# Optimization experiments

Hardware: AMD Instinct MI355X
Metric: run time of the kernel (lower is better)

## Reference

```python
import math
import jax, jax.numpy as jnp
import numpy as np

TOPK = 10
GAMMA = 0.0
DELTA = 0.05
EPS = 1e-8
QR_RANK_EPS = 1e-6
B, D, C = 4096, 2048, 10000


def setup_inputs() -> dict:
    key = jax.random.key(0)
    kz, kw, kn = jax.random.split(key, 3)
    z = jax.random.normal(kz, (B, D), jnp.float32)
    W = jax.random.normal(kw, (C, D), jnp.float32) * 0.02
    logits = z @ W.T                      # (B, C)
    y = jnp.argmax(logits, axis=1)        # correct-class labels -> positive margins
    noise = jax.random.normal(kn, (B, D), jnp.float32)  # one Gaussian draw per sample
    return {"z": z, "y": y, "logits": logits, "W": W, "noise": noise}


def reference(z, y, logits, W, noise):
    # z: (B,D), y: (B,), logits: (B,C), W: (C,D), noise: (B,D)
    b, d = z.shape
    c = W.shape[0]
    k = min(TOPK, c - 1)
    log_term = math.log(1.0 / max(DELTA, 1e-12))

    # top-K confusing classes (exclude true class)
    lm = logits.at[jnp.arange(b), y].set(-1e9)
    _, topk_idx = jax.lax.top_k(lm, k)            # (B, K)

    w_y = W[y]                                    # (B, D)
    w_ks = W[topk_idx]                            # (B, K, D)
    A = w_y[:, None, :] - w_ks                    # (B, K, D) rows = w_y - w_k

    # batched reduced QR of A^T : Q (B,D,K), R (B,K,K)
    Q, R = jnp.linalg.qr(jnp.swapaxes(A, 1, 2))
    keep = jnp.abs(jnp.diagonal(R, axis1=-2, axis2=-1)) > QR_RANK_EPS  # (B, K)
    Qm = Q * keep[:, None, :].astype(Q.dtype)     # zero dropped columns == Q[:, keep]
    valid_basis = keep.any(axis=1)

    # margins and nuisance-projected differences
    margins = jnp.einsum('bkd,bd->bk', A, z)                      # (B, K)
    coef = jnp.einsum('bkd,bdr->bkr', A, Qm)                      # (B, K, K)
    diffs_N = A - jnp.einsum('bkr,bdr->bkd', coef, Qm)            # (B, K, D)
    pn2 = jnp.maximum(jnp.sum(diffs_N * diffs_N, axis=-1), EPS)   # (B, K)
    slack = jnp.maximum(margins - GAMMA, 0.0)
    alpha_k = slack * slack / (2.0 * pn2 * log_term + EPS)
    alpha = jnp.min(alpha_k, axis=1)                              # (B,)

    valid = valid_basis & (alpha > 0.0) & jnp.isfinite(alpha)
    scale = jnp.where(valid, jnp.sqrt(jnp.maximum(alpha, 0.0)), 0.0)

    # project noise onto nuisance subspace and inject
    nc = jnp.einsum('bd,bdr->br', noise, Qm)
    epsN = noise - jnp.einsum('br,bdr->bd', nc, Qm)               # (B, D)
    z_aug = z + jax.lax.stop_gradient(scale[:, None] * epsN)
    # invalid samples carry scale=0 (z_aug == z); `valid` marks real augmentations
    return z_aug, y, valid
```

## Files before the change

### kernel.cpp

```cpp
#include <hip/hip_runtime.h>
#include <math.h>

#define BB 4096
#define DD 2048
#define CC 10000
#define KK 10
#define NT 256
#define NW 4
#define NF4 2500
#define TRI(k) ((k)*((k)+1)/2)

__global__ __launch_bounds__(NT, 6) void topk_kernel(
    const float* __restrict__ logits, const int* __restrict__ y,
    int* __restrict__ topk)
{
    __shared__ float s_cv[NW * KK];
    __shared__ int   s_ci[NW * KK];

    const int b = blockIdx.x, tid = threadIdx.x;
    const int lane = tid & 63, wave = tid >> 6;
    const int yb = y[b];

    float4 lg[10];
    const float4* lrow = (const float4*)(logits + (size_t)b * CC);
    #pragma unroll
    for (int j = 0; j < 10; ++j) {
        const int i4 = tid + 256 * j;
        if (i4 < NF4) lg[j] = lrow[i4];
        else          lg[j] = make_float4(-3e38f, -3e38f, -3e38f, -3e38f);
    }
    #pragma unroll
    for (int j = 0; j < 10; ++j) {
        const int rel = yb - 4 * (tid + 256 * j);
        if (rel == 0) lg[j].x = -3e38f;
        else if (rel == 1) lg[j].y = -3e38f;
        else if (rel == 2) lg[j].z = -3e38f;
        else if (rel == 3) lg[j].w = -3e38f;
    }

    float lbest; int lbidx;
    auto rescan = [&]() {
        lbest = -3.1e38f; lbidx = 0x7fffffff;
        #pragma unroll
        for (int j = 0; j < 10; ++j) {
            const int base = 4 * (tid + 256 * j);
            if (lg[j].x > lbest) { lbest = lg[j].x; lbidx = base + 0; }
            if (lg[j].y > lbest) { lbest = lg[j].y; lbidx = base + 1; }
            if (lg[j].z > lbest) { lbest = lg[j].z; lbidx = base + 2; }
            if (lg[j].w > lbest) { lbest = lg[j].w; lbidx = base + 3; }
        }
    };
    rescan();

    for (int r = 0; r < KK; ++r) {
        float bv = lbest; int bi = lbidx;
        #pragma unroll
        for (int off = 32; off > 0; off >>= 1) {
            const float ov = __shfl_down(bv, off, 64);
            const int   oi = __shfl_down(bi, off, 64);
            if (ov > bv || (ov == bv && oi < bi)) { bv = ov; bi = oi; }
        }
        bv = __shfl(bv, 0, 64);
        bi = __shfl(bi, 0, 64);
        if (lane == 0) { s_cv[wave * KK + r] = bv; s_ci[wave * KK + r] = bi; }
        if (lbidx == bi) {
            const int jw = ((bi >> 2) - tid) >> 8;
            const int cw = bi & 3;
            #pragma unroll
            for (int j = 0; j < 10; ++j) if (j == jw) {
                if (cw == 0) lg[j].x = -3e38f;
                else if (cw == 1) lg[j].y = -3e38f;
                else if (cw == 2) lg[j].z = -3e38f;
                else lg[j].w = -3e38f;
            }
            rescan();
        }
    }
    __syncthreads();

    if (wave == 0) {
        float cv = (lane < NW * KK) ? s_cv[lane] : -3.1e38f;
        int   ci = (lane < NW * KK) ? s_ci[lane] : 0x7fffffff;
        for (int r = 0; r < KK; ++r) {
            float bv = cv; int bi = ci;
            #pragma unroll
            for (int off = 32; off > 0; off >>= 1) {
                const float ov = __shfl_down(bv, off, 64);
                const int   oi = __shfl_down(bi, off, 64);
                if (ov > bv || (ov == bv && oi < bi)) { bv = ov; bi = oi; }
            }
            bi = __shfl(bi, 0, 64);
            if (lane == 0) topk[b * KK + r] = bi;
            if (ci == bi) cv = -3.1e38f;
        }
    }
}

__global__ __launch_bounds__(NT, 3) void aug_kernel(
    const float* __restrict__ z, const int* __restrict__ y,
    const float* __restrict__ W, const float* __restrict__ noise,
    const int* __restrict__ topk, float* __restrict__ out, int write_tail)
{
    __shared__ float s_part[NW][80];
    __shared__ float s_sol[16];

    const int b = blockIdx.x, tid = threadIdx.x;
    const int lane = tid & 63, wave = tid >> 6;
    const int yb = y[b];

    int kidx[KK];
    #pragma unroll
    for (int k = 0; k < KK; ++k) kidx[k] = topk[b * KK + k];

    const size_t zoff = (size_t)b * DD;
    const float4 z0 = ((const float4*)(z + zoff))[tid];
    const float4 z1 = ((const float4*)(z + zoff + 1024))[tid];
    const float4 n0 = ((const float4*)(noise + zoff))[tid];
    const float4 n1 = ((const float4*)(noise + zoff + 1024))[tid];

    float acc[75];
    #pragma unroll
    for (int t = 0; t < 75; ++t) acc[t] = 0.0f;

    const size_t wyo = (size_t)yb * DD;
    #pragma unroll
    for (int c = 0; c < 2; ++c) {
        const size_t coff = (size_t)c * 1024;
        const float4 wy4 = ((const float4*)(W + wyo + coff))[tid];
        float4 a4[KK];
        #pragma unroll
        for (int k = 0; k < KK; ++k) {
            const float4 wk4 = ((const float4*)(W + (size_t)kidx[k] * DD + coff))[tid];
            a4[k].x = wy4.x - wk4.x; a4[k].y = wy4.y - wk4.y;
            a4[k].z = wy4.z - wk4.z; a4[k].w = wy4.w - wk4.w;
        }
        const float4 zc = c ? z1 : z0;
        const float4 nc = c ? n1 : n0;
        const float ze[4] = {zc.x, zc.y, zc.z, zc.w};
        const float ne[4] = {nc.x, nc.y, nc.z, nc.w};
        #pragma unroll
        for (int e = 0; e < 4; ++e) {
            float ak[KK];
            #pragma unroll
            for (int k = 0; k < KK; ++k)
                ak[k] = (e == 0) ? a4[k].x : (e == 1) ? a4[k].y : (e == 2) ? a4[k].z : a4[k].w;
            #pragma unroll
            for (int k = 0; k < KK; ++k) {
                acc[55 + k] += ak[k] * ze[e];
                acc[65 + k] += ak[k] * ne[e];
                #pragma unroll
                for (int j = 0; j <= k; ++j)
                    acc[TRI(k) + j] += ak[j] * ak[k];
            }
        }
    }

    #pragma unroll
    for (int t = 0; t < 75; ++t) {
        float x = acc[t];
        #pragma unroll
        for (int off = 32; off > 0; off >>= 1) x += __shfl_down(x, off, 64);
        if (lane == 0) s_part[wave][t] = x;
    }
    __syncthreads();

    if (wave == 0) {
        float g[75];
        #pragma unroll
        for (int t = 0; t < 75; ++t)
            g[t] = s_part[0][t] + s_part[1][t] + s_part[2][t] + s_part[3][t];

        float dinv[KK];
        unsigned keepmask = 0u;
        #pragma unroll
        for (int k = 0; k < KK; ++k) {
            float s = g[TRI(k) + k];
            #pragma unroll
            for (int j = 0; j < KK; ++j) if (j < k) { const float l = g[TRI(k) + j]; s -= l * l; }
            const float dkk = sqrtf(fmaxf(s, 0.0f));
            const bool kp = dkk > 1e-6f;
            if (kp) keepmask |= (1u << k);
            dinv[k] = kp ? 1.0f / dkk : 0.0f;
            g[TRI(k) + k] = dkk;
            #pragma unroll
            for (int i = 0; i < KK; ++i) if (i > k) {
                float t2 = g[TRI(i) + k];
                #pragma unroll
                for (int j = 0; j < KK; ++j) if (j < k) t2 -= g[TRI(i) + j] * g[TRI(k) + j];
                g[TRI(i) + k] = t2 * dinv[k];
            }
        }
        float cvec[KK];
        #pragma unroll
        for (int i = 0; i < KK; ++i) {
            float s = g[65 + i];
            #pragma unroll
            for (int j = 0; j < KK; ++j) if (j < i) s -= g[TRI(i) + j] * cvec[j];
            cvec[i] = s * dinv[i];
        }
        #pragma unroll
        for (int i = KK - 1; i >= 0; --i) {
            float s = cvec[i];
            #pragma unroll
            for (int j = 0; j < KK; ++j) if (j > i) s -= g[TRI(j) + i] * cvec[j];
            cvec[i] = s * dinv[i];
        }
        const float denomf = 6.9914645e-8f;
        float amin = 3.0e38f;
        #pragma unroll
        for (int k = 0; k < KK; ++k) {
            const float sl = fmaxf(g[55 + k], 0.0f);
            amin = fminf(amin, sl * sl / denomf);
        }
        const bool valid = (keepmask != 0u) && (amin > 0.0f) && isfinite(amin);
        const float scale = valid ? sqrtf(amin) : 0.0f;
        if (lane == 0) {
            #pragma unroll
            for (int k = 0; k < KK; ++k) s_sol[k] = cvec[k];
            s_sol[10] = scale;
            s_sol[11] = valid ? 1.0f : 0.0f;
        }
    }
    __syncthreads();

    float cvec[KK];
    #pragma unroll
    for (int k = 0; k < KK; ++k) cvec[k] = s_sol[k];
    const float scale = s_sol[10];

    #pragma unroll
    for (int c = 0; c < 2; ++c) {
        const size_t coff = (size_t)c * 1024;
        const float4 wy4 = ((const float4*)(W + wyo + coff))[tid];
        float4 proj = make_float4(0.f, 0.f, 0.f, 0.f);
        float csum = 0.f;
        #pragma unroll
        for (int k = 0; k < KK; ++k) {
            const float4 wk4 = ((const float4*)(W + (size_t)kidx[k] * DD + coff))[tid];
            proj.x -= cvec[k] * wk4.x; proj.y -= cvec[k] * wk4.y;
            proj.z -= cvec[k] * wk4.z; proj.w -= cvec[k] * wk4.w;
            csum += cvec[k];
        }
        proj.x += csum * wy4.x; proj.y += csum * wy4.y;
        proj.z += csum * wy4.z; proj.w += csum * wy4.w;
        const float4 zc = c ? z1 : z0;
        const float4 nc = c ? n1 : n0;
        float4 o;
        o.x = zc.x + scale * (nc.x - proj.x);
        o.y = zc.y + scale * (nc.y - proj.y);
        o.z = zc.z + scale * (nc.z - proj.z);
        o.w = zc.w + scale * (nc.w - proj.w);
        ((float4*)(out + zoff + coff))[tid] = o;
    }

    if (write_tail && tid == 0) {
        out[(size_t)BB * DD + b] = (float)yb;
        out[(size_t)BB * DD + BB + b] = s_sol[11];
    }
}

extern "C" void kernel_launch(void* const* d_in, const int* in_sizes, int n_in,
                              void* d_out, int out_size, void* d_ws, size_t ws_size,
                              hipStream_t stream) {
    const float* z      = (const float*)d_in[0];
    const int*   y      = (const int*)d_in[1];
    const float* logits = (const float*)d_in[2];
    const float* W      = (const float*)d_in[3];
    const float* noise  = (const float*)d_in[4];
    float* out = (float*)d_out;
    int* topk = (int*)d_ws;

    topk_kernel<<<BB, NT, 0, stream>>>(logits, y, topk);
    const int write_tail = (out_size >= BB * DD + 2 * BB) ? 1 : 0;
    aug_kernel<<<BB, NT, 0, stream>>>(z, y, W, noise, topk, out, write_tail);
}
```

Baseline: 478.7 us.

## Fuse top-k selection and augmentation into one kernel, keep A rows in registers

Merges the top-k kernel and the augmentation kernel into one per-sample kernel, passing the top-k indices through shared memory instead of a global workspace. The difference rows A are now loaded once and held in registers (80 float4 values) for both the Gram accumulation and the output projection, so the second pass over W is no longer needed. This saves a kernel launch, the global round-trip of the indices, and half of the W gather traffic. The cost is much higher register pressure (launch bounds drop to 2 blocks per SM), which lowers occupancy and may cause spills.

```diff
diff --git a/kernel.cpp b/kernel.cpp
--- a/kernel.cpp
+++ b/kernel.cpp
@@ -10,70 +10,76 @@
 #define NF4 2500
 #define TRI(k) ((k)*((k)+1)/2)
 
-__global__ __launch_bounds__(NT, 6) void topk_kernel(
+__global__ __launch_bounds__(NT, 2) void fused_kernel(
     const float* __restrict__ logits, const int* __restrict__ y,
-    int* __restrict__ topk)
+    const float* __restrict__ z, const float* __restrict__ W,
+    const float* __restrict__ noise, float* __restrict__ out, int write_tail)
 {
     __shared__ float s_cv[NW * KK];
     __shared__ int   s_ci[NW * KK];
+    __shared__ int   s_kidx[KK];
+    __shared__ float s_part[NW][80];
+    __shared__ float s_sol[16];
 
     const int b = blockIdx.x, tid = threadIdx.x;
     const int lane = tid & 63, wave = tid >> 6;
     const int yb = y[b];
 
-    float4 lg[10];
-    const float4* lrow = (const float4*)(logits + (size_t)b * CC);
-    #pragma unroll
-    for (int j = 0; j < 10; ++j) {
-        const int i4 = tid + 256 * j;
-        if (i4 < NF4) lg[j] = lrow[i4];
-        else          lg[j] = make_float4(-3e38f, -3e38f, -3e38f, -3e38f);
-    }
-    #pragma unroll
-    for (int j = 0; j < 10; ++j) {
-        const int rel = yb - 4 * (tid + 256 * j);
-        if (rel == 0) lg[j].x = -3e38f;
-        else if (rel == 1) lg[j].y = -3e38f;
-        else if (rel == 2) lg[j].z = -3e38f;
-        else if (rel == 3) lg[j].w = -3e38f;
-    }
-
-    float lbest; int lbidx;
-    auto rescan = [&]() {
-        lbest = -3.1e38f; lbidx = 0x7fffffff;
+    {
+        float4 lg[10];
+        const float4* lrow = (const float4*)(logits + (size_t)b * CC);
         #pragma unroll
         for (int j = 0; j < 10; ++j) {
-            const int base = 4 * (tid + 256 * j);
-            if (lg[j].x > lbest) { lbest = lg[j].x; lbidx = base + 0; }
-            if (lg[j].y > lbest) { lbest = lg[j].y; lbidx = base + 1; }
-            if (lg[j].z > lbest) { lbest = lg[j].z; lbidx = base + 2; }
-            if (lg[j].w > lbest) { lbest = lg[j].w; lbidx = base + 3; }
-        }
-    };
-    rescan();
-
-    for (int r = 0; r < KK; ++r) {
-        float bv = lbest; int bi = lbidx;
-        #pragma unroll
-        for (int off = 32; off > 0; off >>= 1) {
-            const float ov = __shfl_down(bv, off, 64);
-            const int   oi = __shfl_down(bi, off, 64);
-            if (ov > bv || (ov == bv && oi < bi)) { bv = ov; bi = oi; }
-        }
-        bv = __shfl(bv, 0, 64);
-        bi = __shfl(bi, 0, 64);
-        if (lane == 0) { s_cv[wave * KK + r] = bv; s_ci[wave * KK + r] = bi; }
-        if (lbidx == bi) {
-            const int jw = ((bi >> 2) - tid) >> 8;
-            const int cw = bi & 3;
-            #pragma unroll
-            for (int j = 0; j < 10; ++j) if (j == jw) {
-                if (cw == 0) lg[j].x = -3e38f;
-                else if (cw == 1) lg[j].y = -3e38f;
-                else if (cw == 2) lg[j].z = -3e38f;
-                else lg[j].w = -3e38f;
-            }
-            rescan();
+            const int i4 = tid + 256 * j;
+            if (i4 < NF4) lg[j] = lrow[i4];
+            else          lg[j] = make_float4(-3e38f, -3e38f, -3e38f, -3e38f);
+        }
+        #pragma unroll
+        for (int j = 0; j < 10; ++j) {
+            const int rel = yb - 4 * (tid + 256 * j);
+            if (rel == 0) lg[j].x = -3e38f;
+            else if (rel == 1) lg[j].y = -3e38f;
+            else if (rel == 2) lg[j].z = -3e38f;
+            else if (rel == 3) lg[j].w = -3e38f;
+        }
+
+        float lbest; int lbidx;
+        auto rescan = [&]() {
+            lbest = -3.1e38f; lbidx = 0x7fffffff;
+            #pragma unroll
+            for (int j = 0; j < 10; ++j) {
+                const int base = 4 * (tid + 256 * j);
+                if (lg[j].x > lbest) { lbest = lg[j].x; lbidx = base + 0; }
+                if (lg[j].y > lbest) { lbest = lg[j].y; lbidx = base + 1; }
+                if (lg[j].z > lbest) { lbest = lg[j].z; lbidx = base + 2; }
+                if (lg[j].w > lbest) { lbest = lg[j].w; lbidx = base + 3; }
+            }
+        };
+        rescan();
+
+        for (int r = 0; r < KK; ++r) {
+            float bv = lbest; int bi = lbidx;
+            #pragma unroll
+            for (int off = 32; off > 0; off >>= 1) {
+                const float ov = __shfl_down(bv, off, 64);
+                const int   oi = __shfl_down(bi, off, 64);
+                if (ov > bv || (ov == bv && oi < bi)) { bv = ov; bi = oi; }
+            }
+            bv = __shfl(bv, 0, 64);
+            bi = __shfl(bi, 0, 64);
+            if (lane == 0) { s_cv[wave * KK + r] = bv; s_ci[wave * KK + r] = bi; }
+            if (lbidx == bi) {
+                const int jw = ((bi >> 2) - tid) >> 8;
+                const int cw = bi & 3;
+                #pragma unroll
+                for (int j = 0; j < 10; ++j) if (j == jw) {
+                    if (cw == 0) lg[j].x = -3e38f;
+                    else if (cw == 1) lg[j].y = -3e38f;
+                    else if (cw == 2) lg[j].z = -3e38f;
+                    else lg[j].w = -3e38f;
+                }
+                rescan();
+            }
         }
     }
     __syncthreads();
@@ -90,29 +96,14 @@
                 if (ov > bv || (ov == bv && oi < bi)) { bv = ov; bi = oi; }
             }
             bi = __shfl(bi, 0, 64);
-            if (lane == 0) topk[b * KK + r] = bi;
+            if (lane == 0) s_kidx[r] = bi;
             if (ci == bi) cv = -3.1e38f;
         }
     }
-}
-
-__global__ __launch_bounds__(NT, 3) void aug_kernel(
-    const float* __restrict__ z, const int* __restrict__ y,
-    const float* __restrict__ W, const float* __restrict__ noise,
-    const int* __restrict__ topk, float* __restrict__ out, int write_tail)
-{
-    __shared__ float s_part[NW][80];
-    __shared__ float s_sol[16];
-
-    const int b = blockIdx.x, tid = threadIdx.x;
-    const int lane = tid & 63, wave = tid >> 6;
-    const int yb = y[b];
-
-    int kidx[KK];
-    #pragma unroll
-    for (int k = 0; k < KK; ++k) kidx[k] = topk[b * KK + k];
+    __syncthreads();
 
     const size_t zoff = (size_t)b * DD;
+    const size_t wyo  = (size_t)yb * DD;
     const float4 z0 = ((const float4*)(z + zoff))[tid];
     const float4 z1 = ((const float4*)(z + zoff + 1024))[tid];
     const float4 n0 = ((const float4*)(noise + zoff))[tid];
@@ -122,20 +113,29 @@
     #pragma unroll
     for (int t = 0; t < 75; ++t) acc[t] = 0.0f;
 
-    const size_t wyo = (size_t)yb * DD;
-    #pragma unroll
-    for (int c = 0; c < 2; ++c) {
-        const size_t coff = (size_t)c * 1024;
-        const float4 wy4 = ((const float4*)(W + wyo + coff))[tid];
-        float4 a4[KK];
-        #pragma unroll
-        for (int k = 0; k < KK; ++k) {
-            const float4 wk4 = ((const float4*)(W + (size_t)kidx[k] * DD + coff))[tid];
-            a4[k].x = wy4.x - wk4.x; a4[k].y = wy4.y - wk4.y;
-            a4[k].z = wy4.z - wk4.z; a4[k].w = wy4.w - wk4.w;
-        }
-        const float4 zc = c ? z1 : z0;
-        const float4 nc = c ? n1 : n0;
+    float4 a0[KK], a1[KK];
+    {
+        int kidx[KK];
+        #pragma unroll
+        for (int k = 0; k < KK; ++k) kidx[k] = s_kidx[k];
+
+        const float4 wy0 = ((const float4*)(W + wyo))[tid];
+        #pragma unroll
+        for (int k = 0; k < KK; ++k) {
+            const float4 wk4 = ((const float4*)(W + (size_t)kidx[k] * DD))[tid];
+            a0[k].x = wy0.x - wk4.x; a0[k].y = wy0.y - wk4.y;
+            a0[k].z = wy0.z - wk4.z; a0[k].w = wy0.w - wk4.w;
+        }
+        const float4 wy1 = ((const float4*)(W + wyo + 1024))[tid];
+        #pragma unroll
+        for (int k = 0; k < KK; ++k) {
+            const float4 wk4 = ((const float4*)(W + (size_t)kidx[k] * DD + 1024))[tid];
+            a1[k].x = wy1.x - wk4.x; a1[k].y = wy1.y - wk4.y;
+            a1[k].z = wy1.z - wk4.z; a1[k].w = wy1.w - wk4.w;
+        }
+    }
+
+    auto accum = [&](const float4 (&a)[KK], const float4& zc, const float4& nc) {
         const float ze[4] = {zc.x, zc.y, zc.z, zc.w};
         const float ne[4] = {nc.x, nc.y, nc.z, nc.w};
         #pragma unroll
@@ -143,7 +143,7 @@
             float ak[KK];
             #pragma unroll
             for (int k = 0; k < KK; ++k)
-                ak[k] = (e == 0) ? a4[k].x : (e == 1) ? a4[k].y : (e == 2) ? a4[k].z : a4[k].w;
+                ak[k] = (e == 0) ? a[k].x : (e == 1) ? a[k].y : (e == 2) ? a[k].z : a[k].w;
             #pragma unroll
             for (int k = 0; k < KK; ++k) {
                 acc[55 + k] += ak[k] * ze[e];
@@ -153,7 +153,9 @@
                     acc[TRI(k) + j] += ak[j] * ak[k];
             }
         }
-    }
+    };
+    accum(a0, z0, n0);
+    accum(a1, z1, n1);
 
     #pragma unroll
     for (int t = 0; t < 75; ++t) {
@@ -228,30 +230,23 @@
     for (int k = 0; k < KK; ++k) cvec[k] = s_sol[k];
     const float scale = s_sol[10];
 
-    #pragma unroll
-    for (int c = 0; c < 2; ++c) {
-        const size_t coff = (size_t)c * 1024;
-        const float4 wy4 = ((const float4*)(W + wyo + coff))[tid];
+    auto emit = [&](const float4 (&a)[KK], const float4& zc, const float4& nc,
+                    size_t coff) {
         float4 proj = make_float4(0.f, 0.f, 0.f, 0.f);
-        float csum = 0.f;
-        #pragma unroll
-        for (int k = 0; k < KK; ++k) {
-            const float4 wk4 = ((const float4*)(W + (size_t)kidx[k] * DD + coff))[tid];
-            proj.x -= cvec[k] * wk4.x; proj.y -= cvec[k] * wk4.y;
-            proj.z -= cvec[k] * wk4.z; proj.w -= cvec[k] * wk4.w;
-            csum += cvec[k];
-        }
-        proj.x += csum * wy4.x; proj.y += csum * wy4.y;
-        proj.z += csum * wy4.z; proj.w += csum * wy4.w;
-        const float4 zc = c ? z1 : z0;
-        const float4 nc = c ? n1 : n0;
+        #pragma unroll
+        for (int k = 0; k < KK; ++k) {
+            proj.x += cvec[k] * a[k].x; proj.y += cvec[k] * a[k].y;
+            proj.z += cvec[k] * a[k].z; proj.w += cvec[k] * a[k].w;
+        }
         float4 o;
         o.x = zc.x + scale * (nc.x - proj.x);
         o.y = zc.y + scale * (nc.y - proj.y);
         o.z = zc.z + scale * (nc.z - proj.z);
         o.w = zc.w + scale * (nc.w - proj.w);
         ((float4*)(out + zoff + coff))[tid] = o;
-    }
+    };
+    emit(a0, z0, n0, 0);
+    emit(a1, z1, n1, 1024);
 
     if (write_tail && tid == 0) {
         out[(size_t)BB * DD + b] = (float)yb;
@@ -268,9 +263,7 @@
     const float* W      = (const float*)d_in[3];
     const float* noise  = (const float*)d_in[4];
     float* out = (float*)d_out;
-    int* topk = (int*)d_ws;
-
-    topk_kernel<<<BB, NT, 0, stream>>>(logits, y, topk);
     const int write_tail = (out_size >= BB * DD + 2 * BB) ? 1 : 0;
-    aug_kernel<<<BB, NT, 0, stream>>>(z, y, W, noise, topk, out, write_tail);
+
+    fused_kernel<<<BB, NT, 0, stream>>>(logits, y, z, W, noise, out, write_tail);
 }
```

Result: slower. 617.1 us (+28.9%).

## Split Gram accumulation across waves by output entry to cut registers

Applied to the files above, without the earlier changes.

Each of the four waves now computes a disjoint slice of the 75 Gram/margin/noise dot products over the full D dimension, instead of every thread holding all 75 accumulators. This cuts the accumulator registers per thread, which allows launch bounds to rise from 3 to 4 blocks, and removes the cross-wave partial sum. In exchange, every wave reloads W rows from cache (redundant W traffic, up to 4x reads through L1/L2), and z and noise are re-read in the second pass instead of being kept in registers.

```diff
diff --git a/kernel.cpp b/kernel.cpp
--- a/kernel.cpp
+++ b/kernel.cpp
@@ -10,6 +10,13 @@
 #define NF4 2500
 #define TRI(k) ((k)*((k)+1)/2)
 
+constexpr int PJ[55] = {0, 0,1, 0,1,2, 0,1,2,3, 0,1,2,3,4, 0,1,2,3,4,5,
+                        0,1,2,3,4,5,6, 0,1,2,3,4,5,6,7, 0,1,2,3,4,5,6,7,8,
+                        0,1,2,3,4,5,6,7,8,9};
+constexpr int PK[55] = {0, 1,1, 2,2,2, 3,3,3,3, 4,4,4,4,4, 5,5,5,5,5,5,
+                        6,6,6,6,6,6,6, 7,7,7,7,7,7,7,7, 8,8,8,8,8,8,8,8,8,
+                        9,9,9,9,9,9,9,9,9,9};
+
 __global__ __launch_bounds__(NT, 6) void topk_kernel(
     const float* __restrict__ logits, const int* __restrict__ y,
     int* __restrict__ topk)
@@ -96,12 +103,65 @@
     }
 }
 
-__global__ __launch_bounds__(NT, 3) void aug_kernel(
+template<int LO, int CNT, int NROW, bool WZN>
+__device__ __forceinline__ void pass1_accum(
+    const float* __restrict__ W, const float* __restrict__ z,
+    const float* __restrict__ noise, size_t wyo, size_t zoff,
+    const int* kidx, int lane, float* s_g)
+{
+    float acc[CNT];
+    #pragma unroll
+    for (int t = 0; t < CNT; ++t) acc[t] = 0.0f;
+
+    #pragma unroll 1
+    for (int it = 0; it < 8; ++it) {
+        const int p = lane + (it << 6);
+        const float4 wy4 = ((const float4*)(W + wyo))[p];
+        float4 a4[NROW];
+        #pragma unroll
+        for (int k = 0; k < NROW; ++k) {
+            const float4 wk4 = ((const float4*)(W + (size_t)kidx[k] * DD))[p];
+            a4[k].x = wy4.x - wk4.x; a4[k].y = wy4.y - wk4.y;
+            a4[k].z = wy4.z - wk4.z; a4[k].w = wy4.w - wk4.w;
+        }
+        float4 z4 = make_float4(0.f, 0.f, 0.f, 0.f), n4 = z4;
+        if (WZN) {
+            z4 = ((const float4*)(z + zoff))[p];
+            n4 = ((const float4*)(noise + zoff))[p];
+        }
+        #pragma unroll
+        for (int e = 0; e < 4; ++e) {
+            float ak[NROW];
+            #pragma unroll
+            for (int k = 0; k < NROW; ++k)
+                ak[k] = (e == 0) ? a4[k].x : (e == 1) ? a4[k].y
+                      : (e == 2) ? a4[k].z : a4[k].w;
+            const float ze = (e == 0) ? z4.x : (e == 1) ? z4.y : (e == 2) ? z4.z : z4.w;
+            const float ne = (e == 0) ? n4.x : (e == 1) ? n4.y : (e == 2) ? n4.z : n4.w;
+            #pragma unroll
+            for (int t = 0; t < CNT; ++t) {
+                const int g = LO + t;
+                if (g < 55)      acc[t] += ak[PJ[g < 55 ? g : 0]] * ak[PK[g < 55 ? g : 0]];
+                else if (g < 65) acc[t] += ak[(g - 55) < NROW ? (g - 55) : 0] * ze;
+                else             acc[t] += ak[(g - 65) < NROW ? (g - 65) : 0] * ne;
+            }
+        }
+    }
+    #pragma unroll
+    for (int t = 0; t < CNT; ++t) {
+        float x = acc[t];
+        #pragma unroll
+        for (int off = 32; off > 0; off >>= 1) x += __shfl_down(x, off, 64);
+        if (lane == 0) s_g[LO + t] = x;
+    }
+}
+
+__global__ __launch_bounds__(NT, 4) void aug_kernel(
     const float* __restrict__ z, const int* __restrict__ y,
     const float* __restrict__ W, const float* __restrict__ noise,
     const int* __restrict__ topk, float* __restrict__ out, int write_tail)
 {
-    __shared__ float s_part[NW][80];
+    __shared__ float s_g[80];
     __shared__ float s_sol[16];
 
     const int b = blockIdx.x, tid = threadIdx.x;
@@ -113,62 +173,18 @@
     for (int k = 0; k < KK; ++k) kidx[k] = topk[b * KK + k];
 
     const size_t zoff = (size_t)b * DD;
-    const float4 z0 = ((const float4*)(z + zoff))[tid];
-    const float4 z1 = ((const float4*)(z + zoff + 1024))[tid];
-    const float4 n0 = ((const float4*)(noise + zoff))[tid];
-    const float4 n1 = ((const float4*)(noise + zoff + 1024))[tid];
-
-    float acc[75];
-    #pragma unroll
-    for (int t = 0; t < 75; ++t) acc[t] = 0.0f;
-
-    const size_t wyo = (size_t)yb * DD;
-    #pragma unroll
-    for (int c = 0; c < 2; ++c) {
-        const size_t coff = (size_t)c * 1024;
-        const float4 wy4 = ((const float4*)(W + wyo + coff))[tid];
-        float4 a4[KK];
-        #pragma unroll
-        for (int k = 0; k < KK; ++k) {
-            const float4 wk4 = ((const float4*)(W + (size_t)kidx[k] * DD + coff))[tid];
-            a4[k].x = wy4.x - wk4.x; a4[k].y = wy4.y - wk4.y;
-            a4[k].z = wy4.z - wk4.z; a4[k].w = wy4.w - wk4.w;
-        }
-        const float4 zc = c ? z1 : z0;
-        const float4 nc = c ? n1 : n0;
-        const float ze[4] = {zc.x, zc.y, zc.z, zc.w};
-        const float ne[4] = {nc.x, nc.y, nc.z, nc.w};
-        #pragma unroll
-        for (int e = 0; e < 4; ++e) {
-            float ak[KK];
-            #pragma unroll
-            for (int k = 0; k < KK; ++k)
-                ak[k] = (e == 0) ? a4[k].x : (e == 1) ? a4[k].y : (e == 2) ? a4[k].z : a4[k].w;
-            #pragma unroll
-            for (int k = 0; k < KK; ++k) {
-                acc[55 + k] += ak[k] * ze[e];
-                acc[65 + k] += ak[k] * ne[e];
-                #pragma unroll
-                for (int j = 0; j <= k; ++j)
-                    acc[TRI(k) + j] += ak[j] * ak[k];
-            }
-        }
-    }
-
-    #pragma unroll
-    for (int t = 0; t < 75; ++t) {
-        float x = acc[t];
-        #pragma unroll
-        for (int off = 32; off > 0; off >>= 1) x += __shfl_down(x, off, 64);
-        if (lane == 0) s_part[wave][t] = x;
-    }
+    const size_t wyo  = (size_t)yb * DD;
+
+    if (wave == 0)      pass1_accum< 0, 19,  6, false>(W, z, noise, wyo, zoff, kidx, lane, s_g);
+    else if (wave == 1) pass1_accum<19, 19,  9, false>(W, z, noise, wyo, zoff, kidx, lane, s_g);
+    else if (wave == 2) pass1_accum<38, 17, 10, false>(W, z, noise, wyo, zoff, kidx, lane, s_g);
+    else                pass1_accum<55, 20, 10, true >(W, z, noise, wyo, zoff, kidx, lane, s_g);
     __syncthreads();
 
     if (wave == 0) {
         float g[75];
         #pragma unroll
-        for (int t = 0; t < 75; ++t)
-            g[t] = s_part[0][t] + s_part[1][t] + s_part[2][t] + s_part[3][t];
+        for (int t = 0; t < 75; ++t) g[t] = s_g[t];
 
         float dinv[KK];
         unsigned keepmask = 0u;
@@ -243,8 +259,8 @@
         }
         proj.x += csum * wy4.x; proj.y += csum * wy4.y;
         proj.z += csum * wy4.z; proj.w += csum * wy4.w;
-        const float4 zc = c ? z1 : z0;
-        const float4 nc = c ? n1 : n0;
+        const float4 zc = ((const float4*)(z + zoff + coff))[tid];
+        const float4 nc = ((const float4*)(noise + zoff + coff))[tid];
         float4 o;
         o.x = zc.x + scale * (nc.x - proj.x);
         o.y = zc.y + scale * (nc.y - proj.y);
```

After: 455.4 us. 4.9% less time.
